# Optimization experiments

Hardware: AMD Instinct MI355X
Metric: run time of the kernel (lower is better)

The kernel has to match this reference:

```python
import jax, jax.numpy as jnp
import numpy as np

B = 32        # number of groups (batch.unique())
L = 512       # max_len (equal-size groups in this setup)
E = 512       # embed_dim
H = 8         # num_heads
N = B * L


def setup_inputs() -> dict:
    key = jax.random.key(0)
    k1, k2, k3 = jax.random.split(key, 3)
    embeddings = jax.random.normal(k1, (N, E), dtype=jnp.float32)
    # sorted group ids; equal group sizes keep max_len static for jit
    batch = jnp.repeat(jnp.arange(B, dtype=jnp.int32), L)
    in_proj_w = jax.random.normal(k2, (3 * E, E), dtype=jnp.float32) * (1.0 / np.sqrt(E))
    in_proj_b = jnp.zeros((3 * E,), dtype=jnp.float32)
    out_proj_w = jax.random.normal(k3, (E, E), dtype=jnp.float32) * (1.0 / np.sqrt(E))
    out_proj_b = jnp.zeros((E,), dtype=jnp.float32)
    return {"embeddings": embeddings, "batch": batch,
            "in_proj_w": in_proj_w, "in_proj_b": in_proj_b,
            "out_proj_w": out_proj_w, "out_proj_b": out_proj_b}


def reference(embeddings, batch, in_proj_w, in_proj_b, out_proj_w, out_proj_b):
    Dh = E // H
    ones = jnp.ones_like(batch, dtype=jnp.int32)
    counts = jax.ops.segment_sum(ones, batch, num_segments=B)          # [B]
    starts = jnp.cumsum(counts) - counts                               # exclusive cumsum
    pos = jnp.arange(N, dtype=jnp.int32) - starts[batch]               # position within group
    # pad ragged -> [B, L, E] (zeros for padding, as in torch code)
    padded = jnp.zeros((B, L, E), dtype=embeddings.dtype).at[batch, pos].set(embeddings)
    # FAITHFUL float attn_mask: +1.0 added to scores outside the valid block
    valid = (jnp.arange(L)[None, :] < counts[:, None]).astype(embeddings.dtype)  # [B, L]
    add_mask = 1.0 - valid[:, :, None] * valid[:, None, :]             # [B, Lq, Lk]

    qkv = padded @ in_proj_w.T + in_proj_b                             # [B, L, 3E]
    q, k, v = jnp.split(qkv, 3, axis=-1)
    q = q.reshape(B, L, H, Dh)
    k = k.reshape(B, L, H, Dh)
    v = v.reshape(B, L, H, Dh)
    scale = 1.0 / np.sqrt(Dh)
    scores = jnp.einsum('bqhd,bkhd->bhqk', q, k) * scale + add_mask[:, None, :, :]
    attn = jax.nn.softmax(scores, axis=-1)
    ctx = jnp.einsum('bhqk,bkhd->bqhd', attn, v).reshape(B, L, E)
    attn_out = ctx @ out_proj_w.T + out_proj_b                         # [B, L, E]
    # max_pool1d over sequence (includes padded query rows, as original)
    return jnp.max(attn_out, axis=1)                                   # [B, E]
```

## Files before the change

kernel.cpp:

```cpp
#include <hip/hip_runtime.h>
#include <math.h>


#define B_ 32
#define L_ 512
#define E_ 512
#define H_ 8
#define DH 64
#define N_ (B_ * L_)
#define EMB_N (N_ * E_)
#define IPW_N (3 * E_ * E_)
#define OPW_N (E_ * E_)

typedef _Float16 f16;
typedef __attribute__((ext_vector_type(8))) _Float16 f16x8;
typedef __attribute__((ext_vector_type(4))) float f32x4;
typedef unsigned short u16;

__device__ __forceinline__ u16 f16_bits(float x) {
    f16 h = (f16)x;
    return *reinterpret_cast<u16*>(&h);
}
__device__ __forceinline__ unsigned pk2(float a, float b) {
    return (unsigned)f16_bits(a) | ((unsigned)f16_bits(b) << 16);
}
__device__ __forceinline__ void async16(const void* g, void* l) {
    __builtin_amdgcn_global_load_lds(
        (const __attribute__((address_space(1))) void*)g,
        (__attribute__((address_space(3))) void*)l, 16, 0, 0);
}

__device__ __forceinline__ void atomicMaxFloat(float* addr, float val) {
    if (val >= 0.0f) atomicMax((int*)addr, __float_as_int(val));
    else             atomicMin((unsigned int*)addr, __float_as_uint(val));
}

__global__ __launch_bounds__(256) void cvt_kernel(
        const float* __restrict__ emb, const float* __restrict__ ipw,
        const float* __restrict__ opw,
        u16* __restrict__ eh, u16* __restrict__ wh, u16* __restrict__ oh,
        float* __restrict__ out) {
    if (blockIdx.x < 16) {
        int o = blockIdx.x * 1024 + threadIdx.x * 4;
        float4 ninf = make_float4(-INFINITY, -INFINITY, -INFINITY, -INFINITY);
        *(float4*)(out + o) = ninf;
    }
    size_t i = ((size_t)blockIdx.x * 256 + threadIdx.x) * 8;
    const float* src; u16* dst; size_t off;
    if (i < EMB_N)              { src = emb; dst = eh; off = i; }
    else if (i < EMB_N + IPW_N) { src = ipw; dst = wh; off = i - EMB_N; }
    else                        { src = opw; dst = oh; off = i - EMB_N - IPW_N; }
    float4 a = *(const float4*)(src + off);
    float4 b = *(const float4*)(src + off + 4);
    uint4 p;
    p.x = pk2(a.x, a.y); p.y = pk2(a.z, a.w);
    p.z = pk2(b.x, b.y); p.w = pk2(b.z, b.w);
    *(uint4*)(dst + off) = p;
}

__global__ __launch_bounds__(256) void qkv_mfma(
        const u16* __restrict__ Wg, const u16* __restrict__ Eg,
        const float* __restrict__ bias,
        u16* __restrict__ qg, u16* __restrict__ kg, u16* __restrict__ vg) {
    __shared__ u16 Ah[2][128 * 32], Bh[2][128 * 32];
    const int tok0 = blockIdx.x * 128, row0 = blockIdx.y * 128;
    const int tid = threadIdx.x, wave = tid >> 6, lane = tid & 63;
    const int quad = lane >> 4, c = lane & 15;
    const int wr = (wave >> 1) * 64, wc = (wave & 1) * 64;
    const int sw = (quad ^ ((c >> 1) & 3)) * 8;
    const bool vblk = (row0 >= 1024);

    f32x4 zero = {0.f, 0.f, 0.f, 0.f};
    f32x4 acc[4][4];
#pragma unroll
    for (int i = 0; i < 4; i++)
#pragma unroll
        for (int j = 0; j < 4; j++) acc[i][j] = zero;

    auto stage = [&](int buf, int kt) {
#pragma unroll
        for (int it = 0; it < 2; it++) {
            int chunk = (wave * 2 + it) * 64 + lane;
            int r = chunk >> 2, g = chunk & 3;
            int pos = g ^ ((r >> 1) & 3);
            int lbase = (wave * 2 + it) * 512;
            async16(Wg + (size_t)(row0 + r) * E_ + kt * 32 + pos * 8, &Ah[buf][lbase]);
            async16(Eg + (size_t)(tok0 + r) * E_ + kt * 32 + pos * 8, &Bh[buf][lbase]);
        }
    };

    stage(0, 0);
    for (int kt = 0; kt < 16; kt++) {
        __syncthreads();
        if (kt < 15) stage((kt + 1) & 1, kt + 1);
        const int buf = kt & 1;
        const u16* Mh = vblk ? Bh[buf] : Ah[buf];
        const u16* Nh = vblk ? Ah[buf] : Bh[buf];
        f16x8 mf[4], nf[4];
#pragma unroll
        for (int i = 0; i < 4; i++)
            mf[i] = *(const f16x8*)&Mh[(wr + i * 16 + c) * 32 + sw];
#pragma unroll
        for (int j = 0; j < 4; j++)
            nf[j] = *(const f16x8*)&Nh[(wc + j * 16 + c) * 32 + sw];
#pragma unroll
        for (int i = 0; i < 4; i++)
#pragma unroll
            for (int j = 0; j < 4; j++)
                acc[i][j] = __builtin_amdgcn_mfma_f32_16x16x32_f16(mf[i], nf[j], acc[i][j], 0, 0, 0);
    }

    if (!vblk) {
        const int which = row0 >> 9;
        u16* dst = which ? kg : qg;
        const float scale = which ? 1.0f : 0.18033688f;
        const int h = ((row0 & 511) + wr) >> 6;
#pragma unroll
        for (int i = 0; i < 4; i++) {
            const int d0 = i * 16 + quad * 4;
            float4 bv = *(const float4*)(bias + row0 + wr + d0);
#pragma unroll
            for (int j = 0; j < 4; j++) {
                int n = tok0 + wc + j * 16 + c;
                int bb = n >> 9, l = n & 511;
                uint2 st;
                st.x = pk2((acc[i][j][0] + bv.x) * scale, (acc[i][j][1] + bv.y) * scale);
                st.y = pk2((acc[i][j][2] + bv.z) * scale, (acc[i][j][3] + bv.w) * scale);
                *(uint2*)(dst + (((size_t)(bb * H_ + h)) * L_ + l) * DH + d0) = st;
            }
        }
    } else {
        const int bb = tok0 >> 9;
        const int l0 = (tok0 & 511) + wr;
#pragma unroll
        for (int j = 0; j < 4; j++) {
            int mw = row0 + wc + j * 16 + c;
            int h = (mw & 511) >> 6, d = mw & 63;
            float bv = bias[mw];
#pragma unroll
            for (int i = 0; i < 4; i++) {
                int l = l0 + i * 16 + quad * 4;
                uint2 st;
                st.x = pk2(acc[i][j][0] + bv, acc[i][j][1] + bv);
                st.y = pk2(acc[i][j][2] + bv, acc[i][j][3] + bv);
                *(uint2*)(vg + (((size_t)(bb * H_ + h)) * DH + d) * L_ + l) = st;
            }
        }
    }
}

__global__ __launch_bounds__(256) void attn_mfma(
        const u16* __restrict__ qg, const u16* __restrict__ kg,
        const u16* __restrict__ vg, u16* __restrict__ ctx) {
    __shared__ u16 ks[2][4096];
    __shared__ u16 vt[2][4096];
    __shared__ u16 ps[4][1024];
    const int qt = blockIdx.x, h = blockIdx.y, b = blockIdx.z;
    const int tid = threadIdx.x, wave = tid >> 6, lane = tid & 63;
    const int quad = lane >> 4, c = lane & 15;
    const size_t base = ((size_t)(b * H_ + h)) * (L_ * DH);

    f16x8 qf[2][2];
#pragma unroll
    for (int rs = 0; rs < 2; rs++)
#pragma unroll
        for (int kk = 0; kk < 2; kk++)
            qf[rs][kk] = *(const f16x8*)(qg + base +
                (size_t)(qt * 128 + wave * 32 + rs * 16 + c) * DH + kk * 32 + quad * 8);

    f32x4 zero = {0.f, 0.f, 0.f, 0.f};
    f32x4 Of[2][4];
    float lsum[2] = {0.f, 0.f};
#pragma unroll
    for (int rs = 0; rs < 2; rs++)
#pragma unroll
        for (int j = 0; j < 4; j++) Of[rs][j] = zero;

    auto stage = [&](int buf, int kt) {
#pragma unroll
        for (int it = 0; it < 2; it++) {
            int chunk = (wave * 2 + it) * 64 + lane;
            int r = chunk >> 3, g = chunk & 7;
            int pos = g ^ (r & 7);
            int lbase = (wave * 2 + it) * 512;
            async16(kg + base + (size_t)(kt * 64 + r) * DH + pos * 8, &ks[buf][lbase]);
            async16(vg + base + (size_t)r * L_ + kt * 64 + pos * 8, &vt[buf][lbase]);
        }
    };

    stage(0, 0);
    for (int kt = 0; kt < 8; kt++) {
        __syncthreads();
        if (kt < 7) stage((kt + 1) & 1, kt + 1);
        const int buf = kt & 1;

        f16x8 kf[4][2];
#pragma unroll
        for (int jj = 0; jj < 4; jj++)
#pragma unroll
            for (int kk = 0; kk < 2; kk++)
                kf[jj][kk] = *(const f16x8*)&ks[buf][(jj * 16 + c) * 64 +
                                                    (((kk * 4 + quad) ^ (c & 7)) * 8)];
        f16x8 vf[2][4];
#pragma unroll
        for (int kk = 0; kk < 2; kk++)
#pragma unroll
            for (int j = 0; j < 4; j++)
                vf[kk][j] = *(const f16x8*)&vt[buf][(j * 16 + c) * 64 +
                                                    (((kk * 4 + quad) ^ (c & 7)) * 8)];

#pragma unroll
        for (int rs = 0; rs < 2; rs++) {
            f32x4 Sf[4];
#pragma unroll
            for (int jj = 0; jj < 4; jj++) {
                Sf[jj] = zero;
#pragma unroll
                for (int kk = 0; kk < 2; kk++)
                    Sf[jj] = __builtin_amdgcn_mfma_f32_16x16x32_f16(kf[jj][kk], qf[rs][kk], Sf[jj], 0, 0, 0);
            }
            unsigned pk[4][2];
            float rsum = 0.f;
#pragma unroll
            for (int jj = 0; jj < 4; jj++) {
                float p0 = exp2f(Sf[jj][0] - 6.0f), p1 = exp2f(Sf[jj][1] - 6.0f);
                float p2 = exp2f(Sf[jj][2] - 6.0f), p3 = exp2f(Sf[jj][3] - 6.0f);
                rsum += (p0 + p1) + (p2 + p3);
                pk[jj][0] = pk2(p0, p1);
                pk[jj][1] = pk2(p2, p3);
            }
            lsum[rs] += rsum;

            u16* psw = ps[wave];
#pragma unroll
            for (int jj = 0; jj < 4; jj++) {
                int addr = ((2 * jj + (quad >> 1)) * 16 + c) * 8 + 4 * (quad & 1);
                *(uint2*)&psw[addr] = make_uint2(pk[jj][0], pk[jj][1]);
            }
            f16x8 pf0 = *(const f16x8*)&psw[((0 * 4 + quad) * 16 + c) * 8];
            f16x8 pf1 = *(const f16x8*)&psw[((1 * 4 + quad) * 16 + c) * 8];
#pragma unroll
            for (int j = 0; j < 4; j++) {
                Of[rs][j] = __builtin_amdgcn_mfma_f32_16x16x32_f16(vf[0][j], pf0, Of[rs][j], 0, 0, 0);
                Of[rs][j] = __builtin_amdgcn_mfma_f32_16x16x32_f16(vf[1][j], pf1, Of[rs][j], 0, 0, 0);
            }
        }
    }

#pragma unroll
    for (int rs = 0; rs < 2; rs++) {
        float li = lsum[rs];
        li += __shfl_xor(li, 16);
        li += __shfl_xor(li, 32);
        float inv = 1.0f / li;
        int n = b * L_ + qt * 128 + wave * 32 + rs * 16 + c;
#pragma unroll
        for (int j = 0; j < 4; j++) {
            int d0 = j * 16 + quad * 4;
            uint2 st;
            st.x = pk2(Of[rs][j][0] * inv, Of[rs][j][1] * inv);
            st.y = pk2(Of[rs][j][2] * inv, Of[rs][j][3] * inv);
            *(uint2*)(ctx + (size_t)n * E_ + h * DH + d0) = st;
        }
    }
}

__global__ __launch_bounds__(256) void proj_mfma(
        const u16* __restrict__ Ag, const u16* __restrict__ Bg,
        const float* __restrict__ bias, float* __restrict__ out) {
    __shared__ u16 Ah[2][128 * 32], Bh[2][128 * 32];
    __shared__ float red[2][128];
    const int row0 = blockIdx.x * 128, col0 = blockIdx.y * 128;
    const int tid = threadIdx.x, wave = tid >> 6, lane = tid & 63;
    const int quad = lane >> 4, c = lane & 15;
    const int wr = (wave >> 1) * 64, wc = (wave & 1) * 64;
    const int sw = (quad ^ ((c >> 1) & 3)) * 8;

    f32x4 zero = {0.f, 0.f, 0.f, 0.f};
    f32x4 acc[4][4];
#pragma unroll
    for (int i = 0; i < 4; i++)
#pragma unroll
        for (int j = 0; j < 4; j++) acc[i][j] = zero;

    auto stage = [&](int buf, int kt) {
#pragma unroll
        for (int it = 0; it < 2; it++) {
            int chunk = (wave * 2 + it) * 64 + lane;
            int r = chunk >> 2, g = chunk & 3;
            int pos = g ^ ((r >> 1) & 3);
            int lbase = (wave * 2 + it) * 512;
            async16(Ag + (size_t)(row0 + r) * E_ + kt * 32 + pos * 8, &Ah[buf][lbase]);
            async16(Bg + (size_t)(col0 + r) * E_ + kt * 32 + pos * 8, &Bh[buf][lbase]);
        }
    };

    stage(0, 0);
    for (int kt = 0; kt < 16; kt++) {
        __syncthreads();
        if (kt < 15) stage((kt + 1) & 1, kt + 1);
        const int buf = kt & 1;
        f16x8 af[4], bf[4];
#pragma unroll
        for (int i = 0; i < 4; i++)
            af[i] = *(const f16x8*)&Ah[buf][(wr + i * 16 + c) * 32 + sw];
#pragma unroll
        for (int j = 0; j < 4; j++)
            bf[j] = *(const f16x8*)&Bh[buf][(wc + j * 16 + c) * 32 + sw];
#pragma unroll
        for (int i = 0; i < 4; i++)
#pragma unroll
            for (int j = 0; j < 4; j++)
                acc[i][j] = __builtin_amdgcn_mfma_f32_16x16x32_f16(af[i], bf[j], acc[i][j], 0, 0, 0);
    }

    float cm[4];
#pragma unroll
    for (int j = 0; j < 4; j++) {
        cm[j] = -INFINITY;
#pragma unroll
        for (int i = 0; i < 4; i++)
#pragma unroll
            for (int r = 0; r < 4; r++) cm[j] = fmaxf(cm[j], acc[i][j][r]);
        cm[j] = fmaxf(cm[j], __shfl_xor(cm[j], 16));
        cm[j] = fmaxf(cm[j], __shfl_xor(cm[j], 32));
    }
    if (quad == 0)
#pragma unroll
        for (int j = 0; j < 4; j++) red[wave >> 1][wc + j * 16 + c] = cm[j];
    __syncthreads();
    if (tid < 128) {
        int bb = row0 >> 9;
        float m = fmaxf(red[0][tid], red[1][tid]) + bias[col0 + tid];
        atomicMaxFloat(&out[(size_t)bb * E_ + col0 + tid], m);
    }
}

extern "C" void kernel_launch(void* const* d_in, const int* in_sizes, int n_in,
                              void* d_out, int out_size, void* d_ws, size_t ws_size,
                              hipStream_t stream) {
    const float* emb = (const float*)d_in[0];
    const float* ipw = (const float*)d_in[2];
    const float* ipb = (const float*)d_in[3];
    const float* opw = (const float*)d_in[4];
    const float* opb = (const float*)d_in[5];
    float* out = (float*)d_out;

    u16* eh  = (u16*)d_ws;
    u16* wh  = eh + EMB_N;
    u16* oh  = wh + IPW_N;
    u16* qg  = oh + OPW_N;
    u16* kg  = qg + (size_t)N_ * E_;
    u16* vg  = kg + (size_t)N_ * E_;
    u16* ctx = vg + (size_t)N_ * E_;

    cvt_kernel<<<(EMB_N + IPW_N + OPW_N) / (256 * 8), 256, 0, stream>>>(
        emb, ipw, opw, eh, wh, oh, out);
    qkv_mfma<<<dim3(N_ / 128, (3 * E_) / 128), 256, 0, stream>>>(
        wh, eh, ipb, qg, kg, vg);
    attn_mfma<<<dim3(L_ / 128, H_, B_), 256, 0, stream>>>(qg, kg, vg, ctx);
    proj_mfma<<<dim3(N_ / 128, E_ / 128), 256, 0, stream>>>(ctx, oh, opb, out);
}
```

Measured before the change: 184.2 us.

## Double token tile per block in QKV and attention kernels with 512 threads

The QKV GEMM now processes 256 tokens per block with 8 waves, so each weight tile loaded into shared memory is reused across twice as many tokens. The attention kernel handles 256 query rows per block with 8 waves, so each K/V tile staged in shared memory serves twice as many queries. Both changes aim to cut global and LDS staging traffic per unit of work. The cost is half as many blocks (fewer blocks per CU for latency hiding) and more LDS per block.

Measured after the change: 167.8 us. 8.9% less time.

```diff
diff --git a/kernel.cpp b/kernel.cpp
--- a/kernel.cpp
+++ b/kernel.cpp
@@ -58,15 +58,16 @@
     *(uint4*)(dst + off) = p;
 }
 
-__global__ __launch_bounds__(256) void qkv_mfma(
+__global__ __launch_bounds__(512) void qkv_mfma(
         const u16* __restrict__ Wg, const u16* __restrict__ Eg,
         const float* __restrict__ bias,
         u16* __restrict__ qg, u16* __restrict__ kg, u16* __restrict__ vg) {
-    __shared__ u16 Ah[2][128 * 32], Bh[2][128 * 32];
-    const int tok0 = blockIdx.x * 128, row0 = blockIdx.y * 128;
+    __shared__ u16 Ah[2][128 * 32];
+    __shared__ u16 Bh[2][256 * 32];
+    const int tok0 = blockIdx.x * 256, row0 = blockIdx.y * 128;
     const int tid = threadIdx.x, wave = tid >> 6, lane = tid & 63;
     const int quad = lane >> 4, c = lane & 15;
-    const int wr = (wave >> 1) * 64, wc = (wave & 1) * 64;
+    const int ww = wave & 1, wt = wave >> 1;
     const int sw = (quad ^ ((c >> 1) & 3)) * 8;
     const bool vblk = (row0 >= 1024);
 
@@ -78,14 +79,20 @@
         for (int j = 0; j < 4; j++) acc[i][j] = zero;
 
     auto stage = [&](int buf, int kt) {
-#pragma unroll
-        for (int it = 0; it < 2; it++) {
-            int chunk = (wave * 2 + it) * 64 + lane;
+        {
+            int chunk = wave * 64 + lane;
             int r = chunk >> 2, g = chunk & 3;
             int pos = g ^ ((r >> 1) & 3);
-            int lbase = (wave * 2 + it) * 512;
-            async16(Wg + (size_t)(row0 + r) * E_ + kt * 32 + pos * 8, &Ah[buf][lbase]);
-            async16(Eg + (size_t)(tok0 + r) * E_ + kt * 32 + pos * 8, &Bh[buf][lbase]);
+            async16(Wg + (size_t)(row0 + r) * E_ + kt * 32 + pos * 8,
+                    &Ah[buf][wave * 512]);
+        }
+#pragma unroll
+        for (int it = 0; it < 2; it++) {
+            int chunk = (it * 8 + wave) * 64 + lane;
+            int r = chunk >> 2, g = chunk & 3;
+            int pos = g ^ ((r >> 1) & 3);
+            async16(Eg + (size_t)(tok0 + r) * E_ + kt * 32 + pos * 8,
+                    &Bh[buf][(it * 8 + wave) * 512]);
         }
     };
 
@@ -94,15 +101,22 @@
         __syncthreads();
         if (kt < 15) stage((kt + 1) & 1, kt + 1);
         const int buf = kt & 1;
-        const u16* Mh = vblk ? Bh[buf] : Ah[buf];
-        const u16* Nh = vblk ? Ah[buf] : Bh[buf];
         f16x8 mf[4], nf[4];
-#pragma unroll
-        for (int i = 0; i < 4; i++)
-            mf[i] = *(const f16x8*)&Mh[(wr + i * 16 + c) * 32 + sw];
-#pragma unroll
-        for (int j = 0; j < 4; j++)
-            nf[j] = *(const f16x8*)&Nh[(wc + j * 16 + c) * 32 + sw];
+        if (!vblk) {
+#pragma unroll
+            for (int i = 0; i < 4; i++)
+                mf[i] = *(const f16x8*)&Ah[buf][(ww * 64 + i * 16 + c) * 32 + sw];
+#pragma unroll
+            for (int j = 0; j < 4; j++)
+                nf[j] = *(const f16x8*)&Bh[buf][(wt * 64 + j * 16 + c) * 32 + sw];
+        } else {
+#pragma unroll
+            for (int i = 0; i < 4; i++)
+                mf[i] = *(const f16x8*)&Bh[buf][(wt * 64 + i * 16 + c) * 32 + sw];
+#pragma unroll
+            for (int j = 0; j < 4; j++)
+                nf[j] = *(const f16x8*)&Ah[buf][(ww * 64 + j * 16 + c) * 32 + sw];
+        }
 #pragma unroll
         for (int i = 0; i < 4; i++)
 #pragma unroll
@@ -114,14 +128,14 @@
         const int which = row0 >> 9;
         u16* dst = which ? kg : qg;
         const float scale = which ? 1.0f : 0.18033688f;
-        const int h = ((row0 & 511) + wr) >> 6;
+        const int h = (((row0 & 511) + ww * 64) >> 6);
 #pragma unroll
         for (int i = 0; i < 4; i++) {
             const int d0 = i * 16 + quad * 4;
-            float4 bv = *(const float4*)(bias + row0 + wr + d0);
+            float4 bv = *(const float4*)(bias + row0 + ww * 64 + d0);
 #pragma unroll
             for (int j = 0; j < 4; j++) {
-                int n = tok0 + wc + j * 16 + c;
+                int n = tok0 + wt * 64 + j * 16 + c;
                 int bb = n >> 9, l = n & 511;
                 uint2 st;
                 st.x = pk2((acc[i][j][0] + bv.x) * scale, (acc[i][j][1] + bv.y) * scale);
@@ -131,10 +145,10 @@
         }
     } else {
         const int bb = tok0 >> 9;
-        const int l0 = (tok0 & 511) + wr;
+        const int l0 = (tok0 & 511) + wt * 64;
 #pragma unroll
         for (int j = 0; j < 4; j++) {
-            int mw = row0 + wc + j * 16 + c;
+            int mw = row0 + ww * 64 + j * 16 + c;
             int h = (mw & 511) >> 6, d = mw & 63;
             float bv = bias[mw];
 #pragma unroll
@@ -149,12 +163,12 @@
     }
 }
 
-__global__ __launch_bounds__(256) void attn_mfma(
+__global__ __launch_bounds__(512) void attn_mfma(
         const u16* __restrict__ qg, const u16* __restrict__ kg,
         const u16* __restrict__ vg, u16* __restrict__ ctx) {
     __shared__ u16 ks[2][4096];
     __shared__ u16 vt[2][4096];
-    __shared__ u16 ps[4][1024];
+    __shared__ u16 ps[8][1024];
     const int qt = blockIdx.x, h = blockIdx.y, b = blockIdx.z;
     const int tid = threadIdx.x, wave = tid >> 6, lane = tid & 63;
     const int quad = lane >> 4, c = lane & 15;
@@ -166,7 +180,7 @@
 #pragma unroll
         for (int kk = 0; kk < 2; kk++)
             qf[rs][kk] = *(const f16x8*)(qg + base +
-                (size_t)(qt * 128 + wave * 32 + rs * 16 + c) * DH + kk * 32 + quad * 8);
+                (size_t)(qt * 256 + wave * 32 + rs * 16 + c) * DH + kk * 32 + quad * 8);
 
     f32x4 zero = {0.f, 0.f, 0.f, 0.f};
     f32x4 Of[2][4];
@@ -177,15 +191,11 @@
         for (int j = 0; j < 4; j++) Of[rs][j] = zero;
 
     auto stage = [&](int buf, int kt) {
-#pragma unroll
-        for (int it = 0; it < 2; it++) {
-            int chunk = (wave * 2 + it) * 64 + lane;
-            int r = chunk >> 3, g = chunk & 7;
-            int pos = g ^ (r & 7);
-            int lbase = (wave * 2 + it) * 512;
-            async16(kg + base + (size_t)(kt * 64 + r) * DH + pos * 8, &ks[buf][lbase]);
-            async16(vg + base + (size_t)r * L_ + kt * 64 + pos * 8, &vt[buf][lbase]);
-        }
+        int chunk = wave * 64 + lane;
+        int r = chunk >> 3, g = chunk & 7;
+        int pos = g ^ (r & 7);
+        async16(kg + base + (size_t)(kt * 64 + r) * DH + pos * 8, &ks[buf][wave * 512]);
+        async16(vg + base + (size_t)r * L_ + kt * 64 + pos * 8, &vt[buf][wave * 512]);
     };
 
     stage(0, 0);
@@ -253,7 +263,7 @@
         li += __shfl_xor(li, 16);
         li += __shfl_xor(li, 32);
         float inv = 1.0f / li;
-        int n = b * L_ + qt * 128 + wave * 32 + rs * 16 + c;
+        int n = b * L_ + qt * 256 + wave * 32 + rs * 16 + c;
 #pragma unroll
         for (int j = 0; j < 4; j++) {
             int d0 = j * 16 + quad * 4;
@@ -356,8 +366,8 @@
 
     cvt_kernel<<<(EMB_N + IPW_N + OPW_N) / (256 * 8), 256, 0, stream>>>(
         emb, ipw, opw, eh, wh, oh, out);
-    qkv_mfma<<<dim3(N_ / 128, (3 * E_) / 128), 256, 0, stream>>>(
+    qkv_mfma<<<dim3(N_ / 256, (3 * E_) / 128), 512, 0, stream>>>(
         wh, eh, ipb, qg, kg, vg);
-    attn_mfma<<<dim3(L_ / 128, H_, B_), 256, 0, stream>>>(qg, kg, vg, ctx);
+    attn_mfma<<<dim3(L_ / 256, H_, B_), 512, 0, stream>>>(qg, kg, vg, ctx);
     proj_mfma<<<dim3(N_ / 128, E_ / 128), 256, 0, stream>>>(ctx, oh, opb, out);
 }
```

## Replace LDS-staged async loads with direct global fragment loads in all GEMM/attention kernels

Applied to the files above, without the earlier changes.

Removes the shared-memory double-buffered global_load_lds staging and barriers from the QKV GEMM, attention, and output projection kernels. Each wave now loads its MFMA operand fragments straight from global memory into registers. This drops LDS traffic and __syncthreads, but it loses operand sharing across waves within a block, so global/L2 traffic goes up and memory latency is no longer overlapped by a software pipeline.

After: 279.3 us. 1.52x slower.

```diff
diff --git a/kernel.cpp b/kernel.cpp
--- a/kernel.cpp
+++ b/kernel.cpp
@@ -23,11 +23,6 @@
 }
 __device__ __forceinline__ unsigned pk2(float a, float b) {
     return (unsigned)f16_bits(a) | ((unsigned)f16_bits(b) << 16);
-}
-__device__ __forceinline__ void async16(const void* g, void* l) {
-    __builtin_amdgcn_global_load_lds(
-        (const __attribute__((address_space(1))) void*)g,
-        (__attribute__((address_space(3))) void*)l, 16, 0, 0);
 }
 
 __device__ __forceinline__ void atomicMaxFloat(float* addr, float val) {
@@ -62,13 +57,23 @@
         const u16* __restrict__ Wg, const u16* __restrict__ Eg,
         const float* __restrict__ bias,
         u16* __restrict__ qg, u16* __restrict__ kg, u16* __restrict__ vg) {
-    __shared__ u16 Ah[2][128 * 32], Bh[2][128 * 32];
     const int tok0 = blockIdx.x * 128, row0 = blockIdx.y * 128;
     const int tid = threadIdx.x, wave = tid >> 6, lane = tid & 63;
     const int quad = lane >> 4, c = lane & 15;
     const int wr = (wave >> 1) * 64, wc = (wave & 1) * 64;
-    const int sw = (quad ^ ((c >> 1) & 3)) * 8;
     const bool vblk = (row0 >= 1024);
+
+    const u16* Mg = vblk ? Eg : Wg;
+    const u16* Ng = vblk ? Wg : Eg;
+    const int mrow0 = (vblk ? tok0 : row0) + wr;
+    const int nrow0 = (vblk ? row0 : tok0) + wc;
+    const u16* mp[4];
+    const u16* np[4];
+#pragma unroll
+    for (int i = 0; i < 4; i++) {
+        mp[i] = Mg + (size_t)(mrow0 + i * 16 + c) * E_ + quad * 8;
+        np[i] = Ng + (size_t)(nrow0 + i * 16 + c) * E_ + quad * 8;
+    }
 
     f32x4 zero = {0.f, 0.f, 0.f, 0.f};
     f32x4 acc[4][4];
@@ -77,32 +82,13 @@
 #pragma unroll
         for (int j = 0; j < 4; j++) acc[i][j] = zero;
 
-    auto stage = [&](int buf, int kt) {
-#pragma unroll
-        for (int it = 0; it < 2; it++) {
-            int chunk = (wave * 2 + it) * 64 + lane;
-            int r = chunk >> 2, g = chunk & 3;
-            int pos = g ^ ((r >> 1) & 3);
-            int lbase = (wave * 2 + it) * 512;
-            async16(Wg + (size_t)(row0 + r) * E_ + kt * 32 + pos * 8, &Ah[buf][lbase]);
-            async16(Eg + (size_t)(tok0 + r) * E_ + kt * 32 + pos * 8, &Bh[buf][lbase]);
-        }
-    };
-
-    stage(0, 0);
+#pragma unroll 4
     for (int kt = 0; kt < 16; kt++) {
-        __syncthreads();
-        if (kt < 15) stage((kt + 1) & 1, kt + 1);
-        const int buf = kt & 1;
-        const u16* Mh = vblk ? Bh[buf] : Ah[buf];
-        const u16* Nh = vblk ? Ah[buf] : Bh[buf];
         f16x8 mf[4], nf[4];
 #pragma unroll
-        for (int i = 0; i < 4; i++)
-            mf[i] = *(const f16x8*)&Mh[(wr + i * 16 + c) * 32 + sw];
-#pragma unroll
-        for (int j = 0; j < 4; j++)
-            nf[j] = *(const f16x8*)&Nh[(wc + j * 16 + c) * 32 + sw];
+        for (int i = 0; i < 4; i++) mf[i] = *(const f16x8*)(mp[i] + kt * 32);
+#pragma unroll
+        for (int j = 0; j < 4; j++) nf[j] = *(const f16x8*)(np[j] + kt * 32);
 #pragma unroll
         for (int i = 0; i < 4; i++)
 #pragma unroll
@@ -114,7 +100,7 @@
         const int which = row0 >> 9;
         u16* dst = which ? kg : qg;
         const float scale = which ? 1.0f : 0.18033688f;
-        const int h = ((row0 & 511) + wr) >> 6;
+        const int h = (((row0 & 511) + wr) >> 6);
 #pragma unroll
         for (int i = 0; i < 4; i++) {
             const int d0 = i * 16 + quad * 4;
@@ -152,8 +138,6 @@
 __global__ __launch_bounds__(256) void attn_mfma(
         const u16* __restrict__ qg, const u16* __restrict__ kg,
         const u16* __restrict__ vg, u16* __restrict__ ctx) {
-    __shared__ u16 ks[2][4096];
-    __shared__ u16 vt[2][4096];
     __shared__ u16 ps[4][1024];
     const int qt = blockIdx.x, h = blockIdx.y, b = blockIdx.z;
     const int tid = threadIdx.x, wave = tid >> 6, lane = tid & 63;
@@ -176,38 +160,27 @@
 #pragma unroll
         for (int j = 0; j < 4; j++) Of[rs][j] = zero;
 
-    auto stage = [&](int buf, int kt) {
-#pragma unroll
-        for (int it = 0; it < 2; it++) {
-            int chunk = (wave * 2 + it) * 64 + lane;
-            int r = chunk >> 3, g = chunk & 7;
-            int pos = g ^ (r & 7);
-            int lbase = (wave * 2 + it) * 512;
-            async16(kg + base + (size_t)(kt * 64 + r) * DH + pos * 8, &ks[buf][lbase]);
-            async16(vg + base + (size_t)r * L_ + kt * 64 + pos * 8, &vt[buf][lbase]);
-        }
-    };
-
-    stage(0, 0);
+    const u16* kp[4];
+    const u16* vp[4];
+#pragma unroll
+    for (int i = 0; i < 4; i++) {
+        kp[i] = kg + base + (size_t)(i * 16 + c) * DH + quad * 8;
+        vp[i] = vg + base + (size_t)(i * 16 + c) * L_ + quad * 8;
+    }
+
     for (int kt = 0; kt < 8; kt++) {
-        __syncthreads();
-        if (kt < 7) stage((kt + 1) & 1, kt + 1);
-        const int buf = kt & 1;
-
         f16x8 kf[4][2];
 #pragma unroll
         for (int jj = 0; jj < 4; jj++)
 #pragma unroll
             for (int kk = 0; kk < 2; kk++)
-                kf[jj][kk] = *(const f16x8*)&ks[buf][(jj * 16 + c) * 64 +
-                                                    (((kk * 4 + quad) ^ (c & 7)) * 8)];
+                kf[jj][kk] = *(const f16x8*)(kp[jj] + (size_t)kt * 64 * DH + kk * 32);
         f16x8 vf[2][4];
 #pragma unroll
         for (int kk = 0; kk < 2; kk++)
 #pragma unroll
             for (int j = 0; j < 4; j++)
-                vf[kk][j] = *(const f16x8*)&vt[buf][(j * 16 + c) * 64 +
-                                                    (((kk * 4 + quad) ^ (c & 7)) * 8)];
+                vf[kk][j] = *(const f16x8*)(vp[j] + kt * 64 + kk * 32);
 
 #pragma unroll
         for (int rs = 0; rs < 2; rs++) {
@@ -268,13 +241,19 @@
 __global__ __launch_bounds__(256) void proj_mfma(
         const u16* __restrict__ Ag, const u16* __restrict__ Bg,
         const float* __restrict__ bias, float* __restrict__ out) {
-    __shared__ u16 Ah[2][128 * 32], Bh[2][128 * 32];
     __shared__ float red[2][128];
     const int row0 = blockIdx.x * 128, col0 = blockIdx.y * 128;
     const int tid = threadIdx.x, wave = tid >> 6, lane = tid & 63;
     const int quad = lane >> 4, c = lane & 15;
     const int wr = (wave >> 1) * 64, wc = (wave & 1) * 64;
-    const int sw = (quad ^ ((c >> 1) & 3)) * 8;
+
+    const u16* ap[4];
+    const u16* bp[4];
+#pragma unroll
+    for (int i = 0; i < 4; i++) {
+        ap[i] = Ag + (size_t)(row0 + wr + i * 16 + c) * E_ + quad * 8;
+        bp[i] = Bg + (size_t)(col0 + wc + i * 16 + c) * E_ + quad * 8;
+    }
 
     f32x4 zero = {0.f, 0.f, 0.f, 0.f};
     f32x4 acc[4][4];
@@ -283,30 +262,13 @@
 #pragma unroll
         for (int j = 0; j < 4; j++) acc[i][j] = zero;
 
-    auto stage = [&](int buf, int kt) {
-#pragma unroll
-        for (int it = 0; it < 2; it++) {
-            int chunk = (wave * 2 + it) * 64 + lane;
-            int r = chunk >> 2, g = chunk & 3;
-            int pos = g ^ ((r >> 1) & 3);
-            int lbase = (wave * 2 + it) * 512;
-            async16(Ag + (size_t)(row0 + r) * E_ + kt * 32 + pos * 8, &Ah[buf][lbase]);
-            async16(Bg + (size_t)(col0 + r) * E_ + kt * 32 + pos * 8, &Bh[buf][lbase]);
-        }
-    };
-
-    stage(0, 0);
+#pragma unroll 4
     for (int kt = 0; kt < 16; kt++) {
-        __syncthreads();
-        if (kt < 15) stage((kt + 1) & 1, kt + 1);
-        const int buf = kt & 1;
         f16x8 af[4], bf[4];
 #pragma unroll
-        for (int i = 0; i < 4; i++)
-            af[i] = *(const f16x8*)&Ah[buf][(wr + i * 16 + c) * 32 + sw];
-#pragma unroll
-        for (int j = 0; j < 4; j++)
-            bf[j] = *(const f16x8*)&Bh[buf][(wc + j * 16 + c) * 32 + sw];
+        for (int i = 0; i < 4; i++) af[i] = *(const f16x8*)(ap[i] + kt * 32);
+#pragma unroll
+        for (int j = 0; j < 4; j++) bf[j] = *(const f16x8*)(bp[j] + kt * 32);
 #pragma unroll
         for (int i = 0; i < 4; i++)
 #pragma unroll
```
